# Kernel tuning notes

Measured on AMD Instinct MI355X. Metric: run time of the kernel, lower is better.

## Reference

```python
import jax, jax.numpy as jnp
import numpy as np

N = 100000      # nodes
K = 16          # fixed degree (num_ngbrs)
E = N * K       # edges
NFEAT = 128
NHID = 64
OPFEAT = 64


def setup_inputs() -> dict:
    key = jax.random.key(0)
    ks = jax.random.split(key, 8)
    x = jax.random.normal(ks[0], (N, NFEAT), dtype=jnp.float32)
    # edges sorted by destination node, exactly K per node (required by the
    # original e.view(-1, num_ngbrs) softmax reshape)
    edge_row = jnp.repeat(jnp.arange(N, dtype=jnp.int32), K)
    edge_col = jax.random.randint(ks[1], (E,), 0, N, dtype=jnp.int32)
    stdv1 = 1.0 / np.sqrt(NHID)
    stdv2 = 1.0 / np.sqrt(OPFEAT)
    W1 = jax.random.uniform(ks[2], (NFEAT, NHID), jnp.float32, -stdv1, stdv1)
    b1 = jax.random.uniform(ks[3], (NHID,), jnp.float32, -stdv1, stdv1)
    a1 = jax.random.normal(ks[4], (2 * NHID,), jnp.float32) * 0.1
    W2 = jax.random.uniform(ks[5], (NHID, OPFEAT), jnp.float32, -stdv2, stdv2)
    b2 = jax.random.uniform(ks[6], (OPFEAT,), jnp.float32, -stdv2, stdv2)
    a2 = jax.random.normal(ks[7], (2 * OPFEAT,), jnp.float32) * 0.1
    return {"x": x, "edge_row": edge_row, "edge_col": edge_col,
            "W1": W1, "a1": a1, "b1": b1, "W2": W2, "a2": a2, "b2": b2,
            "k": K}


def _gat_layer(x, W, a, b, edge_row, edge_col, k):
    n = x.shape[0]
    h = x @ W                                        # [N, F_out]
    # edge score: concat(h[dst], h[src]) . a  -> leaky_relu
    h_edge = jnp.concatenate([h[edge_row], h[edge_col]], axis=1)  # [E, 2F]
    e = jax.nn.leaky_relu(h_edge @ a, negative_slope=0.2)         # [E]
    # per-destination softmax over the fixed K neighbors (edges row-sorted)
    att = jax.nn.softmax(e.reshape(-1, k), axis=1).reshape(-1)    # [E]
    att = jax.lax.stop_gradient(att)  # original detaches attention
    # sparse (adj * attention) @ h  ==  segment-sum of att_e * h[src_e]
    out = jax.ops.segment_sum(att[:, None] * h[edge_col], edge_row,
                              num_segments=n)
    return out + b


def reference(x, edge_row, edge_col, W1, a1, b1, W2, a2, b2, k):
    x1 = jax.nn.relu(_gat_layer(x, W1, a1, b1, edge_row, edge_col, k))
    x2 = jax.nn.relu(_gat_layer(x1, W2, a2, b2, edge_row, edge_col, k))
    return x2
```

## Files before the change

kernel.cpp:

```cpp
#include <hip/hip_runtime.h>


typedef __attribute__((ext_vector_type(8))) short bf16x8;
typedef __attribute__((ext_vector_type(4))) float floatx4;

__device__ inline unsigned short f2bf(float x) {
    union { float f; unsigned u; } v; v.f = x;
    unsigned r = v.u + 0x7fff + ((v.u >> 16) & 1);
    return (unsigned short)(r >> 16);
}
__device__ inline float bf2f(unsigned short b) {
    union { float f; unsigned u; } v; v.u = ((unsigned)b) << 16;
    return v.f;
}
__device__ inline void split_bf(float x, unsigned short& h, unsigned short& l) {
    h = f2bf(x);
    l = f2bf(x - bf2f(h));
}
__device__ inline float ubitf(unsigned u) { union { unsigned u; float f; } v; v.u = u; return v.f; }
__device__ inline unsigned fbitu(float f) { union { float f; unsigned u; } v; v.f = f; return v.u; }

__global__ __launch_bounds__(256) void pack_w(
    const float* __restrict__ W1, const float* __restrict__ W2,
    unsigned short* __restrict__ B1hi, unsigned short* __restrict__ B1lo,
    unsigned short* __restrict__ B2hi, unsigned short* __restrict__ B2lo)
{
    int f = blockIdx.x * 256 + threadIdx.x;
    const float* W; unsigned short *hi, *lo;
    if (f < 4096) { W = W1; hi = B1hi; lo = B1lo; }
    else          { f -= 4096; W = W2; hi = B2hi; lo = B2lo; }
    const int ln = f & 63, ntk = f >> 6;
    const int kt = ntk >> 2, nt = ntk & 3;
    const int kbase = kt * 32 + (ln >> 4) * 8;
    const int c = nt * 16 + (ln & 15);
    unsigned short hs[8], ls[8];
#pragma unroll
    for (int j = 0; j < 8; j++) split_bf(W[(kbase + j) * 64 + c], hs[j], ls[j]);
    *(uint4*)&hi[f * 8] = *(const uint4*)hs;
    *(uint4*)&lo[f * 8] = *(const uint4*)ls;
}

template<int KD, int ROWIT>
__global__ __launch_bounds__(256) void gemm_score_mfma(
    const float* __restrict__ X,
    const unsigned short* __restrict__ Bhig, const unsigned short* __restrict__ Blog,
    const float* __restrict__ av, _Float16* __restrict__ H,
    float* __restrict__ s1, float* __restrict__ s2, int n)
{
    constexpr int NKT = KD / 32;
    constexpr int NF = NKT * 4 * 64;
    __shared__ bf16x8 Bhi[NF];
    __shared__ bf16x8 Blo[NF];
    {
        const uint4* sh = (const uint4*)Bhig;
        const uint4* sl = (const uint4*)Blog;
        uint4* dh = (uint4*)Bhi;
        uint4* dl = (uint4*)Blo;
        for (int i = threadIdx.x; i < NF; i += 256) { dh[i] = sh[i]; dl[i] = sl[i]; }
    }
    __syncthreads();

    const int tid = threadIdx.x;
    const int wave = tid >> 6, lane = tid & 63;
    const int quad = lane >> 4, l15 = lane & 15;
    float a1c[4], a2c[4];
#pragma unroll
    for (int nt = 0; nt < 4; nt++) {
        a1c[nt] = av[nt * 16 + l15];
        a2c[nt] = av[64 + nt * 16 + l15];
    }

    for (int it = 0; it < ROWIT; it++) {
        const int r0 = (blockIdx.x * ROWIT + it) * 64 + wave * 16;
        if (r0 >= n) break;
        int ra = r0 + l15; if (ra > n - 1) ra = n - 1;

        bf16x8 Ahi[NKT], Alo[NKT];
#pragma unroll
        for (int kt = 0; kt < NKT; kt++) {
            const uint4 q0 = *(const uint4*)&X[(size_t)ra * KD + kt * 32 + quad * 8];
            const uint4 q1 = *(const uint4*)&X[(size_t)ra * KD + kt * 32 + quad * 8 + 4];
            const unsigned u[8] = {q0.x, q0.y, q0.z, q0.w, q1.x, q1.y, q1.z, q1.w};
            union { bf16x8 v; unsigned w[4]; } ah, al;
#pragma unroll
            for (int i = 0; i < 4; i++) {
                const unsigned a = u[2 * i], b = u[2 * i + 1];
                ah.w[i] = __builtin_amdgcn_perm(b, a, 0x07060302);
                const float ra0 = ubitf(a) - ubitf(a & 0xffff0000u);
                const float rb0 = ubitf(b) - ubitf(b & 0xffff0000u);
                al.w[i] = __builtin_amdgcn_perm(fbitu(rb0), fbitu(ra0), 0x07060302);
            }
            Ahi[kt] = ah.v;
            Alo[kt] = al.v;
        }

        floatx4 acc[4] = {{0,0,0,0},{0,0,0,0},{0,0,0,0},{0,0,0,0}};
#pragma unroll
        for (int kt = 0; kt < NKT; kt++) {
#pragma unroll
            for (int nt = 0; nt < 4; nt++) {
                const int f = (kt * 4 + nt) * 64 + lane;
                const bf16x8 bh = Bhi[f];
                const bf16x8 bl = Blo[f];
                acc[nt] = __builtin_amdgcn_mfma_f32_16x16x32_bf16(Ahi[kt], bh, acc[nt], 0, 0, 0);
                acc[nt] = __builtin_amdgcn_mfma_f32_16x16x32_bf16(Ahi[kt], bl, acc[nt], 0, 0, 0);
                acc[nt] = __builtin_amdgcn_mfma_f32_16x16x32_bf16(Alo[kt], bh, acc[nt], 0, 0, 0);
            }
        }

        float p1[4] = {0,0,0,0}, p2[4] = {0,0,0,0};
#pragma unroll
        for (int nt = 0; nt < 4; nt++) {
#pragma unroll
            for (int reg = 0; reg < 4; reg++) {
                const int r = r0 + quad * 4 + reg;
                if (r < n) H[(size_t)r * 64 + nt * 16 + l15] = (_Float16)acc[nt][reg];
                p1[reg] = fmaf(acc[nt][reg], a1c[nt], p1[reg]);
                p2[reg] = fmaf(acc[nt][reg], a2c[nt], p2[reg]);
            }
        }
#pragma unroll
        for (int m = 1; m < 16; m <<= 1) {
#pragma unroll
            for (int reg = 0; reg < 4; reg++) {
                p1[reg] += __shfl_xor(p1[reg], m, 64);
                p2[reg] += __shfl_xor(p2[reg], m, 64);
            }
        }
        if (l15 == 0) {
#pragma unroll
            for (int reg = 0; reg < 4; reg++) {
                const int r = r0 + quad * 4 + reg;
                if (r < n) { s1[r] = p1[reg]; s2[r] = p2[reg]; }
            }
        }
    }
}

__global__ __launch_bounds__(256) void attn_agg(
    const _Float16* __restrict__ H, const float* __restrict__ s1,
    const float* __restrict__ s2, const int* __restrict__ col,
    const float* __restrict__ bias, float* __restrict__ out, int n)
{
    const int lane = threadIdx.x & 63;
    const int dst = blockIdx.x * 4 + (threadIdx.x >> 6);
    if (dst >= n) return;

    const int c = col[dst * 16 + (lane & 15)];
    float e = s1[dst] + s2[c];
    e = (e > 0.0f) ? e : 0.2f * e;
    float m = e;
#pragma unroll
    for (int msk = 1; msk < 16; msk <<= 1) m = fmaxf(m, __shfl_xor(m, msk, 64));
    float p = __expf(e - m);
    float s = p;
#pragma unroll
    for (int msk = 1; msk < 16; msk <<= 1) s += __shfl_xor(s, msk, 64);
    const float att = p / s;

    int   srck[16];
    float attk[16];
#pragma unroll
    for (int k = 0; k < 16; k++) {
        srck[k] = __shfl(c,   k, 64);
        attk[k] = __shfl(att, k, 64);
    }
    float hv[16];
#pragma unroll
    for (int k = 0; k < 16; k++) hv[k] = (float)H[(size_t)srck[k] * 64 + lane];
    float acc = 0.0f;
#pragma unroll
    for (int k = 0; k < 16; k++) acc = fmaf(attk[k], hv[k], acc);

    const float v = acc + bias[lane];
    out[(size_t)dst * 64 + lane] = fmaxf(v, 0.0f);
}

extern "C" void kernel_launch(void* const* d_in, const int* in_sizes, int n_in,
                              void* d_out, int out_size, void* d_ws, size_t ws_size,
                              hipStream_t stream)
{
    const float* x        = (const float*)d_in[0];
    const int*   edge_col = (const int*)  d_in[2];
    const float* W1       = (const float*)d_in[3];
    const float* a1       = (const float*)d_in[4];
    const float* b1       = (const float*)d_in[5];
    const float* W2       = (const float*)d_in[6];
    const float* a2       = (const float*)d_in[7];
    const float* b2       = (const float*)d_in[8];
    const int n = in_sizes[0] / 128;

    _Float16* h  = (_Float16*)d_ws;
    float* xm = (float*)(h + (size_t)n * 64);
    float* s1 = xm + (size_t)n * 64;
    float* s2 = s1 + n;
    unsigned short* B1hi = (unsigned short*)(s2 + n);
    unsigned short* B1lo = B1hi + 32768;
    unsigned short* B2hi = B1lo + 32768;
    unsigned short* B2lo = B2hi + 16384;

    dim3 blk(256);
    constexpr int ROWIT = 2;
    const int gemm_blocks = (n + ROWIT * 64 - 1) / (ROWIT * 64);
    const int agg_blocks  = (n + 3) / 4;

    pack_w<<<24, blk, 0, stream>>>(W1, W2, B1hi, B1lo, B2hi, B2lo);
    gemm_score_mfma<128, ROWIT><<<gemm_blocks, blk, 0, stream>>>(x, B1hi, B1lo, a1, h, s1, s2, n);
    attn_agg<<<agg_blocks, blk, 0, stream>>>(h, s1, s2, edge_col, b1, xm, n);
    gemm_score_mfma<64, ROWIT><<<gemm_blocks, blk, 0, stream>>>(xm, B2hi, B2lo, a2, h, s1, s2, n);
    attn_agg<<<agg_blocks, blk, 0, stream>>>(h, s1, s2, edge_col, b2, (float*)d_out, n);
}
```

Measured before the change: 218.7 us.

## Inline weight packing, widen GEMM row tiles, vectorize attention gather per quarter-wave

Removes the separate pack_w kernel so each GEMM block splits W into bf16 hi/lo in shared memory itself. Each wave now covers 48 rows (three 16-row sub-tiles), loading all X rows up front and reusing every B fragment read from LDS across three MFMA tiles. The aggregation kernel now gives each destination node a 16-lane group instead of a full wave and gathers 4 fp16 values per lane with ds_bpermute broadcasts and float4 stores. This trades one launch and redundant LDS traffic for higher register pressure (launch bounds of 256,2) and repeated per-block weight conversion.

Result: faster. 190.4 us (-13.0%).

```diff
diff --git a/kernel.cpp b/kernel.cpp
--- a/kernel.cpp
+++ b/kernel.cpp
@@ -3,47 +3,18 @@
 
 typedef __attribute__((ext_vector_type(8))) short bf16x8;
 typedef __attribute__((ext_vector_type(4))) float floatx4;
-
-__device__ inline unsigned short f2bf(float x) {
-    union { float f; unsigned u; } v; v.f = x;
-    unsigned r = v.u + 0x7fff + ((v.u >> 16) & 1);
-    return (unsigned short)(r >> 16);
-}
-__device__ inline float bf2f(unsigned short b) {
-    union { float f; unsigned u; } v; v.u = ((unsigned)b) << 16;
-    return v.f;
-}
-__device__ inline void split_bf(float x, unsigned short& h, unsigned short& l) {
-    h = f2bf(x);
-    l = f2bf(x - bf2f(h));
-}
+typedef __attribute__((ext_vector_type(4))) _Float16 f16x4;
+
 __device__ inline float ubitf(unsigned u) { union { unsigned u; float f; } v; v.u = u; return v.f; }
 __device__ inline unsigned fbitu(float f) { union { float f; unsigned u; } v; v.f = f; return v.u; }
 
-__global__ __launch_bounds__(256) void pack_w(
-    const float* __restrict__ W1, const float* __restrict__ W2,
-    unsigned short* __restrict__ B1hi, unsigned short* __restrict__ B1lo,
-    unsigned short* __restrict__ B2hi, unsigned short* __restrict__ B2lo)
-{
-    int f = blockIdx.x * 256 + threadIdx.x;
-    const float* W; unsigned short *hi, *lo;
-    if (f < 4096) { W = W1; hi = B1hi; lo = B1lo; }
-    else          { f -= 4096; W = W2; hi = B2hi; lo = B2lo; }
-    const int ln = f & 63, ntk = f >> 6;
-    const int kt = ntk >> 2, nt = ntk & 3;
-    const int kbase = kt * 32 + (ln >> 4) * 8;
-    const int c = nt * 16 + (ln & 15);
-    unsigned short hs[8], ls[8];
-#pragma unroll
-    for (int j = 0; j < 8; j++) split_bf(W[(kbase + j) * 64 + c], hs[j], ls[j]);
-    *(uint4*)&hi[f * 8] = *(const uint4*)hs;
-    *(uint4*)&lo[f * 8] = *(const uint4*)ls;
-}
-
-template<int KD, int ROWIT>
-__global__ __launch_bounds__(256) void gemm_score_mfma(
-    const float* __restrict__ X,
-    const unsigned short* __restrict__ Bhig, const unsigned short* __restrict__ Blog,
+__device__ inline unsigned pack_hi16(unsigned a, unsigned b) {
+    return __builtin_amdgcn_perm(b, a, 0x07060302);
+}
+
+template<int KD>
+__global__ __launch_bounds__(256, 2) void gemm_score_mfma(
+    const float* __restrict__ X, const float* __restrict__ W,
     const float* __restrict__ av, _Float16* __restrict__ H,
     float* __restrict__ s1, float* __restrict__ s2, int n)
 {
@@ -51,18 +22,31 @@
     constexpr int NF = NKT * 4 * 64;
     __shared__ bf16x8 Bhi[NF];
     __shared__ bf16x8 Blo[NF];
-    {
-        const uint4* sh = (const uint4*)Bhig;
-        const uint4* sl = (const uint4*)Blog;
-        uint4* dh = (uint4*)Bhi;
-        uint4* dl = (uint4*)Blo;
-        for (int i = threadIdx.x; i < NF; i += 256) { dh[i] = sh[i]; dl[i] = sl[i]; }
+    const int tid = threadIdx.x;
+
+    for (int f = tid; f < NF; f += 256) {
+        const int ln = f & 63, ntk = f >> 6;
+        const int kt = ntk >> 2, nt = ntk & 3;
+        const int kbase = kt * 32 + (ln >> 4) * 8;
+        const int ccol = nt * 16 + (ln & 15);
+        union { bf16x8 v; unsigned w[4]; } hh, ll;
+#pragma unroll
+        for (int i = 0; i < 4; i++) {
+            const unsigned ua = fbitu(W[(kbase + 2 * i) * 64 + ccol]);
+            const unsigned ub = fbitu(W[(kbase + 2 * i + 1) * 64 + ccol]);
+            hh.w[i] = pack_hi16(ua, ub);
+            const float ra = ubitf(ua) - ubitf(ua & 0xffff0000u);
+            const float rb = ubitf(ub) - ubitf(ub & 0xffff0000u);
+            ll.w[i] = pack_hi16(fbitu(ra), fbitu(rb));
+        }
+        Bhi[f] = hh.v; Blo[f] = ll.v;
     }
     __syncthreads();
 
-    const int tid = threadIdx.x;
     const int wave = tid >> 6, lane = tid & 63;
     const int quad = lane >> 4, l15 = lane & 15;
+    const int r0 = blockIdx.x * 192 + wave * 48;
+
     float a1c[4], a2c[4];
 #pragma unroll
     for (int nt = 0; nt < 4; nt++) {
@@ -70,53 +54,68 @@
         a2c[nt] = av[64 + nt * 16 + l15];
     }
 
-    for (int it = 0; it < ROWIT; it++) {
-        const int r0 = (blockIdx.x * ROWIT + it) * 64 + wave * 16;
-        if (r0 >= n) break;
-        int ra = r0 + l15; if (ra > n - 1) ra = n - 1;
-
-        bf16x8 Ahi[NKT], Alo[NKT];
+    uint4 raw[NKT][3][2];
+#pragma unroll
+    for (int rb = 0; rb < 3; rb++) {
+        int ra = r0 + rb * 16 + l15; if (ra > n - 1) ra = n - 1;
+        const float* xp = &X[(size_t)ra * KD + quad * 8];
 #pragma unroll
         for (int kt = 0; kt < NKT; kt++) {
-            const uint4 q0 = *(const uint4*)&X[(size_t)ra * KD + kt * 32 + quad * 8];
-            const uint4 q1 = *(const uint4*)&X[(size_t)ra * KD + kt * 32 + quad * 8 + 4];
-            const unsigned u[8] = {q0.x, q0.y, q0.z, q0.w, q1.x, q1.y, q1.z, q1.w};
+            raw[kt][rb][0] = *(const uint4*)(xp + kt * 32);
+            raw[kt][rb][1] = *(const uint4*)(xp + kt * 32 + 4);
+        }
+    }
+
+    floatx4 acc[4][3];
+#pragma unroll
+    for (int nt = 0; nt < 4; nt++)
+#pragma unroll
+        for (int rb = 0; rb < 3; rb++) acc[nt][rb] = (floatx4){0, 0, 0, 0};
+
+#pragma unroll
+    for (int kt = 0; kt < NKT; kt++) {
+        bf16x8 Ahi[3], Alo[3];
+#pragma unroll
+        for (int rb = 0; rb < 3; rb++) {
+            const unsigned u[8] = {raw[kt][rb][0].x, raw[kt][rb][0].y,
+                                   raw[kt][rb][0].z, raw[kt][rb][0].w,
+                                   raw[kt][rb][1].x, raw[kt][rb][1].y,
+                                   raw[kt][rb][1].z, raw[kt][rb][1].w};
             union { bf16x8 v; unsigned w[4]; } ah, al;
 #pragma unroll
             for (int i = 0; i < 4; i++) {
                 const unsigned a = u[2 * i], b = u[2 * i + 1];
-                ah.w[i] = __builtin_amdgcn_perm(b, a, 0x07060302);
-                const float ra0 = ubitf(a) - ubitf(a & 0xffff0000u);
-                const float rb0 = ubitf(b) - ubitf(b & 0xffff0000u);
-                al.w[i] = __builtin_amdgcn_perm(fbitu(rb0), fbitu(ra0), 0x07060302);
-            }
-            Ahi[kt] = ah.v;
-            Alo[kt] = al.v;
-        }
-
-        floatx4 acc[4] = {{0,0,0,0},{0,0,0,0},{0,0,0,0},{0,0,0,0}};
-#pragma unroll
-        for (int kt = 0; kt < NKT; kt++) {
-#pragma unroll
-            for (int nt = 0; nt < 4; nt++) {
-                const int f = (kt * 4 + nt) * 64 + lane;
-                const bf16x8 bh = Bhi[f];
-                const bf16x8 bl = Blo[f];
-                acc[nt] = __builtin_amdgcn_mfma_f32_16x16x32_bf16(Ahi[kt], bh, acc[nt], 0, 0, 0);
-                acc[nt] = __builtin_amdgcn_mfma_f32_16x16x32_bf16(Ahi[kt], bl, acc[nt], 0, 0, 0);
-                acc[nt] = __builtin_amdgcn_mfma_f32_16x16x32_bf16(Alo[kt], bh, acc[nt], 0, 0, 0);
-            }
-        }
-
-        float p1[4] = {0,0,0,0}, p2[4] = {0,0,0,0};
+                ah.w[i] = pack_hi16(a, b);
+                const float ra = ubitf(a) - ubitf(a & 0xffff0000u);
+                const float rb2 = ubitf(b) - ubitf(b & 0xffff0000u);
+                al.w[i] = pack_hi16(fbitu(ra), fbitu(rb2));
+            }
+            Ahi[rb] = ah.v; Alo[rb] = al.v;
+        }
 #pragma unroll
         for (int nt = 0; nt < 4; nt++) {
+            const bf16x8 bh = Bhi[(kt * 4 + nt) * 64 + lane];
+            const bf16x8 bl = Blo[(kt * 4 + nt) * 64 + lane];
+#pragma unroll
+            for (int rb = 0; rb < 3; rb++) {
+                acc[nt][rb] = __builtin_amdgcn_mfma_f32_16x16x32_bf16(Ahi[rb], bh, acc[nt][rb], 0, 0, 0);
+                acc[nt][rb] = __builtin_amdgcn_mfma_f32_16x16x32_bf16(Ahi[rb], bl, acc[nt][rb], 0, 0, 0);
+                acc[nt][rb] = __builtin_amdgcn_mfma_f32_16x16x32_bf16(Alo[rb], bh, acc[nt][rb], 0, 0, 0);
+            }
+        }
+    }
+
+#pragma unroll
+    for (int rb = 0; rb < 3; rb++) {
+        float p1[4] = {0, 0, 0, 0}, p2[4] = {0, 0, 0, 0};
+#pragma unroll
+        for (int nt = 0; nt < 4; nt++) {
 #pragma unroll
             for (int reg = 0; reg < 4; reg++) {
-                const int r = r0 + quad * 4 + reg;
-                if (r < n) H[(size_t)r * 64 + nt * 16 + l15] = (_Float16)acc[nt][reg];
-                p1[reg] = fmaf(acc[nt][reg], a1c[nt], p1[reg]);
-                p2[reg] = fmaf(acc[nt][reg], a2c[nt], p2[reg]);
+                const int r = r0 + rb * 16 + quad * 4 + reg;
+                if (r < n) H[(size_t)r * 64 + nt * 16 + l15] = (_Float16)acc[nt][rb][reg];
+                p1[reg] = fmaf(acc[nt][rb][reg], a1c[nt], p1[reg]);
+                p2[reg] = fmaf(acc[nt][rb][reg], a2c[nt], p2[reg]);
             }
         }
 #pragma unroll
@@ -130,50 +129,64 @@
         if (l15 == 0) {
 #pragma unroll
             for (int reg = 0; reg < 4; reg++) {
-                const int r = r0 + quad * 4 + reg;
+                const int r = r0 + rb * 16 + quad * 4 + reg;
                 if (r < n) { s1[r] = p1[reg]; s2[r] = p2[reg]; }
             }
         }
     }
 }
 
-__global__ __launch_bounds__(256) void attn_agg(
+__global__ __launch_bounds__(512) void attn_agg(
     const _Float16* __restrict__ H, const float* __restrict__ s1,
     const float* __restrict__ s2, const int* __restrict__ col,
     const float* __restrict__ bias, float* __restrict__ out, int n)
 {
     const int lane = threadIdx.x & 63;
-    const int dst = blockIdx.x * 4 + (threadIdx.x >> 6);
+    const int wv = threadIdx.x >> 6;
+    const int j = lane & 15;
+    const int dst = blockIdx.x * 32 + wv * 4 + (lane >> 4);
     if (dst >= n) return;
 
-    const int c = col[dst * 16 + (lane & 15)];
+    const int c = col[dst * 16 + j];
     float e = s1[dst] + s2[c];
     e = (e > 0.0f) ? e : 0.2f * e;
     float m = e;
 #pragma unroll
-    for (int msk = 1; msk < 16; msk <<= 1) m = fmaxf(m, __shfl_xor(m, msk, 64));
+    for (int mk = 1; mk < 16; mk <<= 1) m = fmaxf(m, __shfl_xor(m, mk, 64));
     float p = __expf(e - m);
     float s = p;
 #pragma unroll
-    for (int msk = 1; msk < 16; msk <<= 1) s += __shfl_xor(s, msk, 64);
+    for (int mk = 1; mk < 16; mk <<= 1) s += __shfl_xor(s, mk, 64);
     const float att = p / s;
 
-    int   srck[16];
-    float attk[16];
+    const int bbase = (lane & 48) << 2;
+    int srck[16]; float attk[16];
 #pragma unroll
     for (int k = 0; k < 16; k++) {
-        srck[k] = __shfl(c,   k, 64);
-        attk[k] = __shfl(att, k, 64);
-    }
-    float hv[16];
-#pragma unroll
-    for (int k = 0; k < 16; k++) hv[k] = (float)H[(size_t)srck[k] * 64 + lane];
-    float acc = 0.0f;
-#pragma unroll
-    for (int k = 0; k < 16; k++) acc = fmaf(attk[k], hv[k], acc);
-
-    const float v = acc + bias[lane];
-    out[(size_t)dst * 64 + lane] = fmaxf(v, 0.0f);
+        const int bidx = bbase + (k << 2);
+        srck[k] = __builtin_amdgcn_ds_bpermute(bidx, c);
+        attk[k] = ubitf((unsigned)__builtin_amdgcn_ds_bpermute(bidx, (int)fbitu(att)));
+    }
+    f16x4 hv[16];
+#pragma unroll
+    for (int k = 0; k < 16; k++)
+        hv[k] = *(const f16x4*)&H[(size_t)srck[k] * 64 + j * 4];
+
+    float a0 = 0, a1 = 0, a2 = 0, a3 = 0;
+#pragma unroll
+    for (int k = 0; k < 16; k++) {
+        a0 = fmaf(attk[k], (float)hv[k][0], a0);
+        a1 = fmaf(attk[k], (float)hv[k][1], a1);
+        a2 = fmaf(attk[k], (float)hv[k][2], a2);
+        a3 = fmaf(attk[k], (float)hv[k][3], a3);
+    }
+    const float4 bv = *(const float4*)&bias[j * 4];
+    float4 o;
+    o.x = fmaxf(a0 + bv.x, 0.0f);
+    o.y = fmaxf(a1 + bv.y, 0.0f);
+    o.z = fmaxf(a2 + bv.z, 0.0f);
+    o.w = fmaxf(a3 + bv.w, 0.0f);
+    *(float4*)&out[(size_t)dst * 64 + j * 4] = o;
 }
 
 extern "C" void kernel_launch(void* const* d_in, const int* in_sizes, int n_in,
@@ -194,19 +207,12 @@
     float* xm = (float*)(h + (size_t)n * 64);
     float* s1 = xm + (size_t)n * 64;
     float* s2 = s1 + n;
-    unsigned short* B1hi = (unsigned short*)(s2 + n);
-    unsigned short* B1lo = B1hi + 32768;
-    unsigned short* B2hi = B1lo + 32768;
-    unsigned short* B2lo = B2hi + 16384;
-
-    dim3 blk(256);
-    constexpr int ROWIT = 2;
-    const int gemm_blocks = (n + ROWIT * 64 - 1) / (ROWIT * 64);
-    const int agg_blocks  = (n + 3) / 4;
-
-    pack_w<<<24, blk, 0, stream>>>(W1, W2, B1hi, B1lo, B2hi, B2lo);
-    gemm_score_mfma<128, ROWIT><<<gemm_blocks, blk, 0, stream>>>(x, B1hi, B1lo, a1, h, s1, s2, n);
-    attn_agg<<<agg_blocks, blk, 0, stream>>>(h, s1, s2, edge_col, b1, xm, n);
-    gemm_score_mfma<64, ROWIT><<<gemm_blocks, blk, 0, stream>>>(xm, B2hi, B2lo, a2, h, s1, s2, n);
-    attn_agg<<<agg_blocks, blk, 0, stream>>>(h, s1, s2, edge_col, b2, (float*)d_out, n);
-}
+
+    const int gemm_blocks = (n + 191) / 192;
+    const int agg_blocks  = (n + 31) / 32;
+
+    gemm_score_mfma<128><<<gemm_blocks, 256, 0, stream>>>(x, W1, a1, h, s1, s2, n);
+    attn_agg<<<agg_blocks, 512, 0, stream>>>(h, s1, s2, edge_col, b1, xm, n);
+    gemm_score_mfma<64><<<gemm_blocks, 256, 0, stream>>>(xm, W2, a2, h, s1, s2, n);
+    attn_agg<<<agg_blocks, 512, 0, stream>>>(h, s1, s2, edge_col, b2, (float*)d_out, n);
+}
```
